# Kernel optimization log

Measured on AMD Instinct MI355X. Metric: run time of the kernel, lower is better.

## Reference

```python
import jax, jax.numpy as jnp
import numpy as np

K = 20  # kNN neighbours (conf.k)

def knn_edge_feats(x, k):
    """x: [B, C, N] -> edge features [B, 2C, N, k] (central || neighbor-central)."""
    xt = jnp.swapaxes(x, 1, 2)                       # [B, N, C]
    sq = jnp.sum(xt * xt, axis=2, keepdims=True)     # [B, N, 1]
    dist = -2.0 * jnp.einsum('bnc,bcm->bnm', xt, x) + sq + jnp.swapaxes(sq, 1, 2)  # [B,N,N]
    idx = jnp.argsort(dist, axis=2)[:, :, 1:k + 1]   # [B, N, k], skip self (col 0)
    nbrs = jax.vmap(lambda xb, ib: xb[:, ib])(x, idx)  # [B, C, N, k]
    central = x[:, :, :, None]                        # [B, C, N, 1]
    return jnp.concatenate([jnp.broadcast_to(central, nbrs.shape), nbrs - central], axis=1)

def edge_conv(x, w, b, k):
    """1x1 conv over edge features, max over k.  x:[B,C,N], w:[Fout,2C], b:[Fout]."""
    ee = knn_edge_feats(x, k)                                   # [B, 2C, N, k]
    y = jnp.einsum('oc,bcnk->bonk', w, ee) + b[None, :, None, None]
    return jnp.max(y, axis=3)                                   # [B, Fout, N]

def setup_inputs() -> dict:
    key = jax.random.key(0)
    ks = iter(jax.random.split(key, 32))
    B, N = 16, 2048
    d = {}
    d['x'] = jax.random.normal(next(ks), (B, 3, N), dtype=jnp.float32)
    def w(shape, scale):
        return jax.random.normal(next(ks), shape, dtype=jnp.float32) * scale
    d['ec0_w'] = w((64, 6), 0.3);    d['ec0_b'] = w((64,), 0.05)
    d['ec1_w'] = w((64, 128), 0.08); d['ec1_b'] = w((64,), 0.05)
    d['ec2_w'] = w((64, 128), 0.08); d['ec2_b'] = w((64,), 0.05)
    d['ec3_w'] = w((128, 128), 0.08); d['ec3_b'] = w((128,), 0.05)
    d['conv0_w'] = w((1024, 320), 0.05); d['conv0_b'] = w((1024,), 0.05)
    d['conv0_s'] = jax.random.uniform(next(ks), (1024,), minval=0.5, maxval=1.5)
    d['conv0_t'] = w((1024,), 0.05)
    d['fc0_w'] = w((512, 1024), 0.03); d['fc0_b'] = w((512,), 0.05)
    d['fc0_s'] = jax.random.uniform(next(ks), (512,), minval=0.5, maxval=1.5)
    d['fc0_t'] = w((512,), 0.05)
    d['fc1_w'] = w((256, 512), 0.04); d['fc1_b'] = w((256,), 0.05)
    d['fc1_s'] = jax.random.uniform(next(ks), (256,), minval=0.5, maxval=1.5)
    d['fc1_t'] = w((256,), 0.05)
    d['fc2_w'] = w((40, 256), 0.06); d['fc2_b'] = w((40,), 0.05)
    d['fc2_s'] = jax.random.uniform(next(ks), (40,), minval=0.5, maxval=1.5)
    d['fc2_t'] = w((40,), 0.05)
    return d

def reference(x, ec0_w, ec0_b, ec1_w, ec1_b, ec2_w, ec2_b, ec3_w, ec3_b,
              conv0_w, conv0_b, conv0_s, conv0_t,
              fc0_w, fc0_b, fc0_s, fc0_t,
              fc1_w, fc1_b, fc1_s, fc1_t,
              fc2_w, fc2_b, fc2_s, fc2_t):
    x1 = edge_conv(x, ec0_w, ec0_b, K)    # [B, 64, N]
    x2 = edge_conv(x1, ec1_w, ec1_b, K)   # [B, 64, N]
    x3 = edge_conv(x2, ec2_w, ec2_b, K)   # [B, 64, N]
    x4 = edge_conv(x3, ec3_w, ec3_b, K)   # [B, 128, N]
    h = jnp.concatenate([x1, x2, x3, x4], axis=1)              # [B, 320, N]
    # conv1dbr: 1x1 conv + BN(affine folded into s,t) + ReLU
    h = jnp.einsum('oc,bcn->bon', conv0_w, h) + conv0_b[None, :, None]
    h = jax.nn.relu(h * conv0_s[None, :, None] + conv0_t[None, :, None])  # [B, 1024, N]
    g = jnp.max(h, axis=2)                                     # [B, 1024]
    # fcbr blocks: linear + BN + ReLU
    g = jax.nn.relu((g @ fc0_w.T + fc0_b) * fc0_s + fc0_t)     # [B, 512]
    g = jax.nn.relu((g @ fc1_w.T + fc1_b) * fc1_s + fc1_t)     # [B, 256]
    g = jax.nn.relu((g @ fc2_w.T + fc2_b) * fc2_s + fc2_t)     # [B, 40]
    return g
```

## Files before the change

kernel.cpp:

```cpp
#include <hip/hip_runtime.h>

#define DEVINL __device__ __forceinline__

static const int NPTS = 2048;

typedef __attribute__((ext_vector_type(8))) short bf16x8;
typedef __attribute__((ext_vector_type(4))) float f32x4;

DEVINL unsigned fenc(float x) {
    int b = __float_as_int(x);
    return (b < 0) ? ~(unsigned)b : ((unsigned)b | 0x80000000u);
}
DEVINL float fdec(unsigned u) {
    return (u & 0x80000000u) ? __int_as_float((int)(u & 0x7fffffffu))
                             : __int_as_float((int)~u);
}
DEVINL unsigned long long u64min(unsigned long long a, unsigned long long b) {
    return (b < a) ? b : a;
}
DEVINL unsigned short f2bf(float x) {
    unsigned u = __float_as_uint(x);
    return (unsigned short)((u + 0x7fffu + ((u >> 16) & 1u)) >> 16);
}
DEVINL float bf2f(unsigned short h) { return __uint_as_float(((unsigned)h) << 16); }

DEVINL void topk20(float v[32], unsigned long long* cand, int lane,
                   int* __restrict__ Iout, int outBase) {
    float t16[16];
#pragma unroll
    for (int i = 0; i < 16; ++i) t16[i] = fminf(v[i], v[i + 16]);
#pragma unroll
    for (int i = 0; i < 8; ++i) t16[i] = fminf(t16[i], t16[i + 8]);
#pragma unroll
    for (int i = 0; i < 4; ++i) t16[i] = fminf(t16[i], t16[i + 4]);
    float s = fminf(fminf(t16[0], t16[1]), fminf(t16[2], t16[3]));
#pragma unroll
    for (int k = 2; k <= 64; k <<= 1) {
#pragma unroll
        for (int j = k >> 1; j >= 1; j >>= 1) {
            float o = __shfl_xor(s, j);
            bool keepmin = (((lane & j) == 0) == ((lane & k) == 0));
            s = keepmin ? fminf(s, o) : fmaxf(s, o);
        }
    }
    const float tau = __shfl(s, 19);
    int cnt = 0;
#pragma unroll
    for (int j = 0; j < 32; ++j) {
        bool pass = (v[j] <= tau);
        unsigned long long mask = __ballot(pass);
        if (pass) {
            int pos = cnt + (int)__popcll(mask & ((1ull << lane) - 1ull));
            if (pos < 64) {
                int col = lane * 4 + (j & 3) + ((j >> 2) << 8);
                cand[pos] = ((unsigned long long)fenc(v[j]) << 32) | (unsigned)col;
            }
        }
        cnt += (int)__popcll(mask);
    }
    if (cnt <= 64) {
        unsigned long long key = (lane < cnt) ? cand[lane] : ~0ull;
#pragma unroll
        for (int k = 2; k <= 64; k <<= 1) {
#pragma unroll
            for (int j = k >> 1; j >= 1; j >>= 1) {
                unsigned long long o = __shfl_xor(key, j);
                bool keepmin = (((lane & j) == 0) == ((lane & k) == 0));
                unsigned long long mn = u64min(key, o);
                unsigned long long mx = (key ^ o) ^ mn;
                key = keepmin ? mn : mx;
            }
        }
        if (lane < 20) Iout[outBase + lane] = (int)(unsigned)(key & 0xffffffffu);
    } else {
        unsigned long long vk[32];
#pragma unroll
        for (int j = 0; j < 32; ++j) {
            int col = lane * 4 + (j & 3) + ((j >> 2) << 8);
            vk[j] = ((unsigned long long)fenc(v[j]) << 32) | (unsigned)col;
        }
        unsigned long long last = 0ull;
        for (int it = 0; it < 20; ++it) {
            unsigned long long q16[16];
#pragma unroll
            for (int i = 0; i < 16; ++i) {
                unsigned long long a = (vk[i] > last) ? vk[i] : ~0ull;
                unsigned long long c = (vk[i + 16] > last) ? vk[i + 16] : ~0ull;
                q16[i] = u64min(a, c);
            }
#pragma unroll
            for (int i = 0; i < 8; ++i) q16[i] = u64min(q16[i], q16[i + 8]);
#pragma unroll
            for (int i = 0; i < 4; ++i) q16[i] = u64min(q16[i], q16[i + 4]);
            unsigned long long best = u64min(u64min(q16[0], q16[1]), u64min(q16[2], q16[3]));
#pragma unroll
            for (int off = 32; off >= 1; off >>= 1) {
                unsigned long long o = __shfl_down(best, off);
                best = u64min(best, o);
            }
            best = __shfl(best, 0);
            if (lane == 0) Iout[outBase + it] = (int)(unsigned)(best & 0xffffffffu);
            last = best;
        }
    }
}

__global__ __launch_bounds__(512, 4) void knnfused_kernel(const float* __restrict__ X, int bs,
                                                          int* __restrict__ Iout) {
    extern __shared__ char smem[];
    float* Dr = (float*)smem;
    float* As = (float*)(smem + 65536);
    unsigned long long* cand = (unsigned long long*)(smem + 67584);
    const int N = NPTS, K = 20;
    const int b = blockIdx.y, n0 = blockIdx.x * 8;
    const float* __restrict__ Xb = X + (size_t)b * bs;
    const int tid = threadIdx.x;
    if (tid < 128) {
        int c = tid >> 1, r4 = (tid & 1) * 4;
        *(float4*)&As[c * 8 + r4] = *(const float4*)&Xb[(size_t)c * N + n0 + r4];
    }
    __syncthreads();
    const int m0 = tid * 4;
    float acc[8][4], sq[4];
#pragma unroll
    for (int r = 0; r < 8; ++r)
#pragma unroll
        for (int j = 0; j < 4; ++j) acc[r][j] = 0.f;
#pragma unroll
    for (int j = 0; j < 4; ++j) sq[j] = 0.f;
#pragma unroll 4
    for (int c = 0; c < 64; ++c) {
        float4 b0 = *(const float4*)&Xb[(size_t)c * N + m0];
        float4 a0 = *(const float4*)&As[c * 8];
        float4 a1 = *(const float4*)&As[c * 8 + 4];
        sq[0] += b0.x * b0.x; sq[1] += b0.y * b0.y;
        sq[2] += b0.z * b0.z; sq[3] += b0.w * b0.w;
        float av[8] = {a0.x, a0.y, a0.z, a0.w, a1.x, a1.y, a1.z, a1.w};
#pragma unroll
        for (int r = 0; r < 8; ++r) {
            acc[r][0] += av[r] * b0.x; acc[r][1] += av[r] * b0.y;
            acc[r][2] += av[r] * b0.z; acc[r][3] += av[r] * b0.w;
        }
    }
    const float INF = __builtin_inff();
#pragma unroll
    for (int r = 0; r < 8; ++r) {
        const int n = n0 + r;
        float d0[4] = {sq[0] - 2.f * acc[r][0], sq[1] - 2.f * acc[r][1],
                       sq[2] - 2.f * acc[r][2], sq[3] - 2.f * acc[r][3]};
#pragma unroll
        for (int j = 0; j < 4; ++j) {
            if (m0 + j == n) d0[j] = INF;
        }
        *(float4*)&Dr[r * N + m0] = make_float4(d0[0], d0[1], d0[2], d0[3]);
    }
    __syncthreads();
    const int w = tid >> 6, lane = tid & 63;
    const float* __restrict__ rp = &Dr[w * N];
    float v[32];
#pragma unroll
    for (int q = 0; q < 8; ++q) {
        float4 x4 = *(const float4*)&rp[lane * 4 + q * 256];
        v[q * 4 + 0] = x4.x; v[q * 4 + 1] = x4.y;
        v[q * 4 + 2] = x4.z; v[q * 4 + 3] = x4.w;
    }
    topk20(v, cand + w * 64, lane, Iout, (b * N + n0 + w) * K);
}

__global__ __launch_bounds__(256) void select0_kernel(const float* __restrict__ X,
                                                      int* __restrict__ Iout) {
    const int N = NPTS, K = 20;
    __shared__ unsigned long long cand[4][64];
    const int w = threadIdx.x >> 6, lane = threadIdx.x & 63;
    const int rowg = blockIdx.x * 4 + w;
    const int b = rowg >> 11, n = rowg & 2047;
    const float* __restrict__ Xb = X + (size_t)b * 3 * N;
    const float xr = Xb[n], yr = Xb[N + n], zr = Xb[2 * N + n];
    const float INF = __builtin_inff();
    float v[32];
#pragma unroll
    for (int q = 0; q < 8; ++q) {
        const int base = lane * 4 + q * 256;
        const float4 xm = *(const float4*)&Xb[base];
        const float4 ym = *(const float4*)&Xb[N + base];
        const float4 zm = *(const float4*)&Xb[2 * N + base];
        float mx[4] = {xm.x, xm.y, xm.z, xm.w};
        float my[4] = {ym.x, ym.y, ym.z, ym.w};
        float mz[4] = {zm.x, zm.y, zm.z, zm.w};
#pragma unroll
        for (int j = 0; j < 4; ++j) {
            float sq = mx[j] * mx[j] + my[j] * my[j] + mz[j] * mz[j];
            float dot = xr * mx[j] + yr * my[j] + zr * mz[j];
            float d = sq - 2.f * dot;
            v[q * 4 + j] = (base + j == n) ? INF : d;
        }
    }
    topk20(v, &cand[w][0], lane, Iout, (b * N + n) * K);
}

template<int F, int C>
__global__ __launch_bounds__(256) void ut_kernel(const float* __restrict__ X, int bs,
                                                 const float* __restrict__ W,
                                                 const float* __restrict__ bias,
                                                 float* __restrict__ U, float* __restrict__ T) {
    const int N = NPTS;
    __shared__ float Ws2[64][C + 1];
    __shared__ float Wsd[64][C + 1];
    const int n0 = blockIdx.x * 64, f0 = blockIdx.y * 64, b = blockIdx.z;
    const int tid = threadIdx.x;
    for (int i = tid; i < 64 * C; i += 256) {
        int ff = i / C, c = i - ff * C;
        float w1 = W[(f0 + ff) * (2 * C) + c];
        float w2 = W[(f0 + ff) * (2 * C) + C + c];
        Ws2[ff][c] = w2;
        Wsd[ff][c] = w1 - w2;
    }
    __syncthreads();
    const int nt = tid & 15, fg = tid >> 4;
    const float* __restrict__ Xb = X + (size_t)b * bs;
    float au[4][4], av[4][4];
#pragma unroll
    for (int i = 0; i < 4; ++i)
#pragma unroll
        for (int j = 0; j < 4; ++j) { au[i][j] = 0.f; av[i][j] = 0.f; }
#pragma unroll 4
    for (int c = 0; c < C; ++c) {
        const float4 xv = *(const float4*)&Xb[(size_t)c * N + n0 + nt * 4];
#pragma unroll
        for (int fi = 0; fi < 4; ++fi) {
            float w2v = Ws2[fg * 4 + fi][c];
            float wdv = Wsd[fg * 4 + fi][c];
            au[fi][0] += w2v * xv.x; au[fi][1] += w2v * xv.y;
            au[fi][2] += w2v * xv.z; au[fi][3] += w2v * xv.w;
            av[fi][0] += wdv * xv.x; av[fi][1] += wdv * xv.y;
            av[fi][2] += wdv * xv.z; av[fi][3] += wdv * xv.w;
        }
    }
#pragma unroll
    for (int ni = 0; ni < 4; ++ni) {
        int n = n0 + nt * 4 + ni;
        float4 uv = make_float4(au[0][ni], au[1][ni], au[2][ni], au[3][ni]);
        *(float4*)&U[((size_t)b * N + n) * F + f0 + fg * 4] = uv;
    }
#pragma unroll
    for (int fi = 0; fi < 4; ++fi) {
        int f = f0 + fg * 4 + fi;
        float bv = bias[f];
        float4 tv = make_float4(av[fi][0] + bv, av[fi][1] + bv, av[fi][2] + bv, av[fi][3] + bv);
        *(float4*)&T[((size_t)b * F + f) * N + n0 + nt * 4] = tv;
    }
}

template<int F, bool WRITE_F32>
__global__ __launch_bounds__(256) void gathermax_kernel(const float* __restrict__ U,
                                                        const float* __restrict__ T,
                                                        const int* __restrict__ idx,
                                                        float* __restrict__ Y, int bsY,
                                                        unsigned short* __restrict__ HtH,
                                                        unsigned short* __restrict__ HtL,
                                                        int hoff) {
    const int N = NPTS, K = 20, FG = F / 8;
    __shared__ int sidx[32 * 20];
    const int b = blockIdx.y, n0 = blockIdx.x * 32, tid = threadIdx.x;
    const int p = tid >> 3, fg = tid & 7;
    for (int t = tid; t < 32 * K; t += 256) sidx[t] = idx[(b * N + n0) * K + t];
    __syncthreads();
    const int n = n0 + p;
    const float* __restrict__ Ub = U + (size_t)b * N * F;
    const int fbase = fg * FG;
    float mx[FG];
#pragma unroll
    for (int i = 0; i < FG; ++i) mx[i] = -__builtin_inff();
#pragma unroll 4
    for (int j = 0; j < K; ++j) {
        const int r = sidx[p * K + j];
        const float4* up = (const float4*)&Ub[(size_t)r * F + fbase];
#pragma unroll
        for (int q = 0; q < FG / 4; ++q) {
            float4 a = up[q];
            mx[q * 4 + 0] = fmaxf(mx[q * 4 + 0], a.x);
            mx[q * 4 + 1] = fmaxf(mx[q * 4 + 1], a.y);
            mx[q * 4 + 2] = fmaxf(mx[q * 4 + 2], a.z);
            mx[q * 4 + 3] = fmaxf(mx[q * 4 + 3], a.w);
        }
    }
    float val[FG];
#pragma unroll
    for (int i = 0; i < FG; ++i) {
        const int f = fbase + i;
        val[i] = T[((size_t)b * F + f) * N + n] + mx[i];
        if (WRITE_F32) Y[(size_t)b * bsY + (size_t)f * N + n] = val[i];
    }
    unsigned short hs[FG], ls[FG];
#pragma unroll
    for (int i = 0; i < FG; ++i) {
        unsigned short h = f2bf(val[i]);
        hs[i] = h;
        ls[i] = f2bf(val[i] - bf2f(h));
    }
    const size_t hb = ((size_t)b * N + n) * 320 + hoff + fbase;
#pragma unroll
    for (int q = 0; q < FG / 8; ++q) {
        *(int4*)&HtH[hb + q * 8] = *(const int4*)&hs[q * 8];
        *(int4*)&HtL[hb + q * 8] = *(const int4*)&ls[q * 8];
    }
}

__global__ __launch_bounds__(256) void wsplit_kernel(const float* __restrict__ W,
                                                     unsigned short* __restrict__ WH,
                                                     unsigned short* __restrict__ WL) {
    const int e = blockIdx.x * 256 + threadIdx.x;
    float w = W[e];
    unsigned short h = f2bf(w);
    WH[e] = h;
    WL[e] = f2bf(w - bf2f(h));
}

__global__ __launch_bounds__(256) void conv0mfma_kernel(const unsigned short* __restrict__ HtH,
                                                        const unsigned short* __restrict__ HtL,
                                                        const unsigned short* __restrict__ WH,
                                                        const unsigned short* __restrict__ WL,
                                                        unsigned* __restrict__ M) {
    const int N = NPTS;
    __shared__ unsigned short HsH[64][40], HsL[64][40], WsH[128][40], WsL[128][40];
    const int n0 = blockIdx.x * 64, f0 = blockIdx.y * 128, b = blockIdx.z;
    const int tid = threadIdx.x;
    const int wave = tid >> 6, lane = tid & 63;
    const int wm = wave & 1, wf = wave >> 1;
    const int row = lane & 15, quad = lane >> 4;
    f32x4 acc[2][4];
#pragma unroll
    for (int i = 0; i < 2; ++i)
#pragma unroll
        for (int j = 0; j < 4; ++j) acc[i][j] = (f32x4){0.f, 0.f, 0.f, 0.f};

    const int hn = tid >> 2, hq = tid & 3;
    const int wfr = tid >> 1, wq = tid & 1;

    for (int c0 = 0; c0 < 320; c0 += 32) {
        {
            const size_t src = ((size_t)b * N + n0 + hn) * 320 + c0 + hq * 8;
            *(int4*)&HsH[hn][hq * 8] = *(const int4*)&HtH[src];
            *(int4*)&HsL[hn][hq * 8] = *(const int4*)&HtL[src];
        }
        {
            const size_t src = (size_t)(f0 + wfr) * 320 + c0 + wq * 16;
            *(int4*)&WsH[wfr][wq * 16]     = *(const int4*)&WH[src];
            *(int4*)&WsH[wfr][wq * 16 + 8] = *(const int4*)&WH[src + 8];
            *(int4*)&WsL[wfr][wq * 16]     = *(const int4*)&WL[src];
            *(int4*)&WsL[wfr][wq * 16 + 8] = *(const int4*)&WL[src + 8];
        }
        __syncthreads();
        bf16x8 aH[2], aL[2];
#pragma unroll
        for (int mt = 0; mt < 2; ++mt) {
            aH[mt] = *(const bf16x8*)&HsH[wm * 32 + mt * 16 + row][quad * 8];
            aL[mt] = *(const bf16x8*)&HsL[wm * 32 + mt * 16 + row][quad * 8];
        }
#pragma unroll
        for (int nt = 0; nt < 4; ++nt) {
            bf16x8 bH = *(const bf16x8*)&WsH[wf * 64 + nt * 16 + row][quad * 8];
            bf16x8 bL = *(const bf16x8*)&WsL[wf * 64 + nt * 16 + row][quad * 8];
#pragma unroll
            for (int mt = 0; mt < 2; ++mt) {
                acc[mt][nt] = __builtin_amdgcn_mfma_f32_16x16x32_bf16(aH[mt], bH, acc[mt][nt], 0, 0, 0);
                acc[mt][nt] = __builtin_amdgcn_mfma_f32_16x16x32_bf16(aH[mt], bL, acc[mt][nt], 0, 0, 0);
                acc[mt][nt] = __builtin_amdgcn_mfma_f32_16x16x32_bf16(aL[mt], bH, acc[mt][nt], 0, 0, 0);
            }
        }
        __syncthreads();
    }
#pragma unroll
    for (int nt = 0; nt < 4; ++nt) {
        float m = acc[0][nt][0];
#pragma unroll
        for (int r = 1; r < 4; ++r) m = fmaxf(m, acc[0][nt][r]);
#pragma unroll
        for (int r = 0; r < 4; ++r) m = fmaxf(m, acc[1][nt][r]);
        m = fmaxf(m, __shfl_down(m, 16));
        m = fmaxf(m, __shfl_down(m, 32));
        if (quad == 0)
            atomicMax(&M[(b << 10) + f0 + wf * 64 + nt * 16 + row], fenc(m));
    }
}

__global__ __launch_bounds__(256) void fc_kernel(const unsigned* __restrict__ M,
    const float* __restrict__ cb, const float* __restrict__ cs, const float* __restrict__ ct,
    const float* __restrict__ w0, const float* __restrict__ b0, const float* __restrict__ s0, const float* __restrict__ t0,
    const float* __restrict__ w1, const float* __restrict__ b1, const float* __restrict__ s1, const float* __restrict__ t1,
    const float* __restrict__ w2, const float* __restrict__ b2, const float* __restrict__ s2, const float* __restrict__ t2,
    float* __restrict__ out) {
    __shared__ float g0[1024], g1[512], g2[256];
    const int b = blockIdx.x, tid = threadIdx.x;
    for (int f = tid; f < 1024; f += 256) {
        float z = fdec(M[b * 1024 + f]);
        float g = cs[f] * (z + cb[f]) + ct[f];
        g0[f] = fmaxf(g, 0.f);
    }
    __syncthreads();
    for (int f = tid; f < 512; f += 256) {
        const float4* wp = (const float4*)(w0 + (size_t)f * 1024);
        float acc = 0.f;
#pragma unroll 4
        for (int c = 0; c < 256; ++c) {
            float4 wv = wp[c];
            float4 gv = *(const float4*)&g0[c * 4];
            acc += wv.x * gv.x + wv.y * gv.y + wv.z * gv.z + wv.w * gv.w;
        }
        float g = s0[f] * (acc + b0[f]) + t0[f];
        g1[f] = fmaxf(g, 0.f);
    }
    __syncthreads();
    if (tid < 256) {
        const float4* wp = (const float4*)(w1 + (size_t)tid * 512);
        float acc = 0.f;
#pragma unroll 4
        for (int c = 0; c < 128; ++c) {
            float4 wv = wp[c];
            float4 gv = *(const float4*)&g1[c * 4];
            acc += wv.x * gv.x + wv.y * gv.y + wv.z * gv.z + wv.w * gv.w;
        }
        float g = s1[tid] * (acc + b1[tid]) + t1[tid];
        g2[tid] = fmaxf(g, 0.f);
    }
    __syncthreads();
    if (tid < 40) {
        const float4* wp = (const float4*)(w2 + (size_t)tid * 256);
        float acc = 0.f;
#pragma unroll 4
        for (int c = 0; c < 64; ++c) {
            float4 wv = wp[c];
            float4 gv = *(const float4*)&g2[c * 4];
            acc += wv.x * gv.x + wv.y * gv.y + wv.z * gv.z + wv.w * gv.w;
        }
        float g = s2[tid] * (acc + b2[tid]) + t2[tid];
        out[b * 40 + tid] = fmaxf(g, 0.f);
    }
}

extern "C" void kernel_launch(void* const* d_in, const int* in_sizes, int n_in,
                              void* d_out, int out_size, void* d_ws, size_t ws_size,
                              hipStream_t stream) {
    const float* x       = (const float*)d_in[0];
    const float* ec0_w   = (const float*)d_in[1];
    const float* ec0_b   = (const float*)d_in[2];
    const float* ec1_w   = (const float*)d_in[3];
    const float* ec1_b   = (const float*)d_in[4];
    const float* ec2_w   = (const float*)d_in[5];
    const float* ec2_b   = (const float*)d_in[6];
    const float* ec3_w   = (const float*)d_in[7];
    const float* ec3_b   = (const float*)d_in[8];
    const float* conv0_w = (const float*)d_in[9];
    const float* conv0_b = (const float*)d_in[10];
    const float* conv0_s = (const float*)d_in[11];
    const float* conv0_t = (const float*)d_in[12];
    const float* fc0_w   = (const float*)d_in[13];
    const float* fc0_b   = (const float*)d_in[14];
    const float* fc0_s   = (const float*)d_in[15];
    const float* fc0_t   = (const float*)d_in[16];
    const float* fc1_w   = (const float*)d_in[17];
    const float* fc1_b   = (const float*)d_in[18];
    const float* fc1_s   = (const float*)d_in[19];
    const float* fc1_t   = (const float*)d_in[20];
    const float* fc2_w   = (const float*)d_in[21];
    const float* fc2_b   = (const float*)d_in[22];
    const float* fc2_s   = (const float*)d_in[23];
    const float* fc2_t   = (const float*)d_in[24];
    float* out = (float*)d_out;

    char* ws = (char*)d_ws;
    const int B = 16, N = NPTS;
    float* Hc   = (float*)(ws + 0);
    float* U    = (float*)(ws + 41943040);
    float* T    = (float*)(ws + 58720256);
    int*   I    = (int*)  (ws + 75497472);
    unsigned* M = (unsigned*)(ws + 78118912);
    unsigned short* W_hi = (unsigned short*)(ws + 78184448);
    unsigned short* W_lo = (unsigned short*)(ws + 78839808);
    unsigned short* HtH  = (unsigned short*)(ws + 79495168);
    unsigned short* HtL  = (unsigned short*)(ws + 100466688);

    (void)hipFuncSetAttribute((const void*)knnfused_kernel,
                              hipFuncAttributeMaxDynamicSharedMemorySize, 71680);

    dim3 blk(256);
    const int bsX0 = 3 * N, bsH = 320 * N;

    wsplit_kernel<<<dim3(1024 * 320 / 256), blk, 0, stream>>>(conv0_w, W_hi, W_lo);

    select0_kernel<<<dim3(B * N / 4), blk, 0, stream>>>(x, I);
    ut_kernel<64, 3><<<dim3(N / 64, 1, B), blk, 0, stream>>>(x, bsX0, ec0_w, ec0_b, U, T);
    gathermax_kernel<64, true><<<dim3(N / 32, B), blk, 0, stream>>>(U, T, I, Hc, bsH, HtH, HtL, 0);

    const float* Xin[3] = {Hc, Hc + (size_t)64 * N, Hc + (size_t)128 * N};
    const float* ecw[3] = {ec1_w, ec2_w, ec3_w};
    const float* ecb[3] = {ec1_b, ec2_b, ec3_b};
    for (int L = 0; L < 3; ++L) {
        knnfused_kernel<<<dim3(N / 8, B), dim3(512), 71680, stream>>>(Xin[L], bsH, I);
        if (L < 2) {
            ut_kernel<64, 64><<<dim3(N / 64, 1, B), blk, 0, stream>>>(Xin[L], bsH, ecw[L], ecb[L], U, T);
            gathermax_kernel<64, true><<<dim3(N / 32, B), blk, 0, stream>>>(
                U, T, I, Hc + (size_t)(64 * (L + 1)) * N, bsH, HtH, HtL, 64 * (L + 1));
        } else {
            ut_kernel<128, 64><<<dim3(N / 64, 2, B), blk, 0, stream>>>(Xin[L], bsH, ecw[L], ecb[L], U, T);
            gathermax_kernel<128, false><<<dim3(N / 32, B), blk, 0, stream>>>(
                U, T, I, Hc + (size_t)192 * N, bsH, HtH, HtL, 192);
        }
    }

    (void)hipMemsetAsync(M, 0, B * 1024 * sizeof(unsigned), stream);
    conv0mfma_kernel<<<dim3(N / 64, 1024 / 128, B), blk, 0, stream>>>(HtH, HtL, W_hi, W_lo, M);

    fc_kernel<<<dim3(B), blk, 0, stream>>>(M, conv0_b, conv0_s, conv0_t,
                                           fc0_w, fc0_b, fc0_s, fc0_t,
                                           fc1_w, fc1_b, fc1_s, fc1_t,
                                           fc2_w, fc2_b, fc2_s, fc2_t, out);
}
```

Measured before the change: 1.035 ms.

## Process 16 query rows per kNN block and use 32-bit top-k fallback

The fused kNN kernel now computes distances for 16 query points per block instead of 8, so each global load of the point tile is reused across twice as many rows and half as many blocks are launched. The second 8 rows are held in registers and written to shared memory after the first top-k pass, reusing the same shared buffer. The fallback top-k loop replaces 64-bit packed key comparisons with 32-bit value plus column tracking and a taken-bitmask. The cost is higher register pressure (64 accumulators plus the 32 held distances), which may lower occupancy, and two sequential top-k passes per warp.

```diff
diff --git a/kernel.cpp b/kernel.cpp
--- a/kernel.cpp
+++ b/kernel.cpp
@@ -73,34 +73,33 @@
         }
         if (lane < 20) Iout[outBase + lane] = (int)(unsigned)(key & 0xffffffffu);
     } else {
-        unsigned long long vk[32];
-#pragma unroll
-        for (int j = 0; j < 32; ++j) {
-            int col = lane * 4 + (j & 3) + ((j >> 2) << 8);
-            vk[j] = ((unsigned long long)fenc(v[j]) << 32) | (unsigned)col;
-        }
-        unsigned long long last = 0ull;
+        unsigned vu[32];
+#pragma unroll
+        for (int j = 0; j < 32; ++j) vu[j] = fenc(v[j]);
+        unsigned taken = 0u;
         for (int it = 0; it < 20; ++it) {
-            unsigned long long q16[16];
-#pragma unroll
-            for (int i = 0; i < 16; ++i) {
-                unsigned long long a = (vk[i] > last) ? vk[i] : ~0ull;
-                unsigned long long c = (vk[i + 16] > last) ? vk[i + 16] : ~0ull;
-                q16[i] = u64min(a, c);
+            unsigned bk = 0xffffffffu;
+            int bc = 0x7fffffff, bj = 0;
+#pragma unroll
+            for (int j = 0; j < 32; ++j) {
+                const int col = lane * 4 + (j & 3) + ((j >> 2) << 8);
+                bool avail = ((taken >> j) & 1u) == 0u;
+                bool better = avail && (vu[j] < bk || (vu[j] == bk && col < bc));
+                bk = better ? vu[j] : bk;
+                bc = better ? col : bc;
+                bj = better ? j : bj;
             }
-#pragma unroll
-            for (int i = 0; i < 8; ++i) q16[i] = u64min(q16[i], q16[i + 8]);
-#pragma unroll
-            for (int i = 0; i < 4; ++i) q16[i] = u64min(q16[i], q16[i + 4]);
-            unsigned long long best = u64min(u64min(q16[0], q16[1]), u64min(q16[2], q16[3]));
+            const int lbc = bc;
 #pragma unroll
             for (int off = 32; off >= 1; off >>= 1) {
-                unsigned long long o = __shfl_down(best, off);
-                best = u64min(best, o);
+                unsigned ok = __shfl_xor(bk, off);
+                int oc = __shfl_xor(bc, off);
+                bool t = (ok < bk) || (ok == bk && oc < bc);
+                bk = t ? ok : bk;
+                bc = t ? oc : bc;
             }
-            best = __shfl(best, 0);
-            if (lane == 0) Iout[outBase + it] = (int)(unsigned)(best & 0xffffffffu);
-            last = best;
+            if (lane == 0) Iout[outBase + it] = bc;
+            if (lbc == bc) taken |= (1u << bj);
         }
     }
 }
@@ -110,20 +109,20 @@
     extern __shared__ char smem[];
     float* Dr = (float*)smem;
     float* As = (float*)(smem + 65536);
-    unsigned long long* cand = (unsigned long long*)(smem + 67584);
+    unsigned long long* cand = (unsigned long long*)(smem + 69632);
     const int N = NPTS, K = 20;
-    const int b = blockIdx.y, n0 = blockIdx.x * 8;
+    const int b = blockIdx.y, n0 = blockIdx.x * 16;
     const float* __restrict__ Xb = X + (size_t)b * bs;
     const int tid = threadIdx.x;
-    if (tid < 128) {
-        int c = tid >> 1, r4 = (tid & 1) * 4;
-        *(float4*)&As[c * 8 + r4] = *(const float4*)&Xb[(size_t)c * N + n0 + r4];
+    if (tid < 256) {
+        int c = tid >> 2, r4 = (tid & 3) * 4;
+        *(float4*)&As[c * 16 + r4] = *(const float4*)&Xb[(size_t)c * N + n0 + r4];
     }
     __syncthreads();
     const int m0 = tid * 4;
-    float acc[8][4], sq[4];
-#pragma unroll
-    for (int r = 0; r < 8; ++r)
+    float acc[16][4], sq[4];
+#pragma unroll
+    for (int r = 0; r < 16; ++r)
 #pragma unroll
         for (int j = 0; j < 4; ++j) acc[r][j] = 0.f;
 #pragma unroll
@@ -131,13 +130,16 @@
 #pragma unroll 4
     for (int c = 0; c < 64; ++c) {
         float4 b0 = *(const float4*)&Xb[(size_t)c * N + m0];
-        float4 a0 = *(const float4*)&As[c * 8];
-        float4 a1 = *(const float4*)&As[c * 8 + 4];
+        float4 a0 = *(const float4*)&As[c * 16];
+        float4 a1 = *(const float4*)&As[c * 16 + 4];
+        float4 a2 = *(const float4*)&As[c * 16 + 8];
+        float4 a3 = *(const float4*)&As[c * 16 + 12];
         sq[0] += b0.x * b0.x; sq[1] += b0.y * b0.y;
         sq[2] += b0.z * b0.z; sq[3] += b0.w * b0.w;
-        float av[8] = {a0.x, a0.y, a0.z, a0.w, a1.x, a1.y, a1.z, a1.w};
-#pragma unroll
-        for (int r = 0; r < 8; ++r) {
+        float av[16] = {a0.x, a0.y, a0.z, a0.w, a1.x, a1.y, a1.z, a1.w,
+                        a2.x, a2.y, a2.z, a2.w, a3.x, a3.y, a3.z, a3.w};
+#pragma unroll
+        for (int r = 0; r < 16; ++r) {
             acc[r][0] += av[r] * b0.x; acc[r][1] += av[r] * b0.y;
             acc[r][2] += av[r] * b0.z; acc[r][3] += av[r] * b0.w;
         }
@@ -154,6 +156,16 @@
         }
         *(float4*)&Dr[r * N + m0] = make_float4(d0[0], d0[1], d0[2], d0[3]);
     }
+    float dd[8][4];
+#pragma unroll
+    for (int r = 0; r < 8; ++r) {
+        const int n = n0 + 8 + r;
+#pragma unroll
+        for (int j = 0; j < 4; ++j) {
+            float d = sq[j] - 2.f * acc[8 + r][j];
+            dd[r][j] = (m0 + j == n) ? INF : d;
+        }
+    }
     __syncthreads();
     const int w = tid >> 6, lane = tid & 63;
     const float* __restrict__ rp = &Dr[w * N];
@@ -164,7 +176,20 @@
         v[q * 4 + 0] = x4.x; v[q * 4 + 1] = x4.y;
         v[q * 4 + 2] = x4.z; v[q * 4 + 3] = x4.w;
     }
+    __syncthreads();
+#pragma unroll
+    for (int r = 0; r < 8; ++r) {
+        *(float4*)&Dr[r * N + m0] = make_float4(dd[r][0], dd[r][1], dd[r][2], dd[r][3]);
+    }
     topk20(v, cand + w * 64, lane, Iout, (b * N + n0 + w) * K);
+    __syncthreads();
+#pragma unroll
+    for (int q = 0; q < 8; ++q) {
+        float4 x4 = *(const float4*)&rp[lane * 4 + q * 256];
+        v[q * 4 + 0] = x4.x; v[q * 4 + 1] = x4.y;
+        v[q * 4 + 2] = x4.z; v[q * 4 + 3] = x4.w;
+    }
+    topk20(v, cand + w * 64, lane, Iout, (b * N + n0 + 8 + w) * K);
 }
 
 __global__ __launch_bounds__(256) void select0_kernel(const float* __restrict__ X,
@@ -481,7 +506,7 @@
     unsigned short* HtL  = (unsigned short*)(ws + 100466688);
 
     (void)hipFuncSetAttribute((const void*)knnfused_kernel,
-                              hipFuncAttributeMaxDynamicSharedMemorySize, 71680);
+                              hipFuncAttributeMaxDynamicSharedMemorySize, 73728);
 
     dim3 blk(256);
     const int bsX0 = 3 * N, bsH = 320 * N;
@@ -496,7 +521,7 @@
     const float* ecw[3] = {ec1_w, ec2_w, ec3_w};
     const float* ecb[3] = {ec1_b, ec2_b, ec3_b};
     for (int L = 0; L < 3; ++L) {
-        knnfused_kernel<<<dim3(N / 8, B), dim3(512), 71680, stream>>>(Xin[L], bsH, I);
+        knnfused_kernel<<<dim3(N / 16, B), dim3(512), 73728, stream>>>(Xin[L], bsH, I);
         if (L < 2) {
             ut_kernel<64, 64><<<dim3(N / 64, 1, B), blk, 0, stream>>>(Xin[L], bsH, ecw[L], ecb[L], U, T);
             gathermax_kernel<64, true><<<dim3(N / 32, B), blk, 0, stream>>>(
```

Result: faster. 966.9 us (-6.6%).
